# Kernel tuning notes

Measured on AMD Instinct MI355X. Metric: run time of the kernel, lower is better.

The kernel has to match this reference:

```python
import jax, jax.numpy as jnp
import numpy as np

B, T, D, H, E, L = 128, 200, 256, 4, 4, 2
HD = D // H
ITEM = 50000


def _ln(x, s, b):
    m = x.mean(-1, keepdims=True)
    v = ((x - m) ** 2).mean(-1, keepdims=True)
    return (x - m) / jnp.sqrt(v + 1e-8) * s + b


def setup_inputs() -> dict:
    key = jax.random.key(0)
    ks = jax.random.split(key, 20)
    n = lambda k, sh: jax.random.normal(k, sh, jnp.float32) * 0.02
    inp = {}
    inp['log_seqs'] = jax.random.randint(ks[0], (B, T), 0, ITEM + 1)
    inp['pos_seqs'] = jax.random.randint(ks[1], (B, T), 0, ITEM + 1)
    inp['neg_seqs'] = jax.random.randint(ks[2], (B, T), 0, ITEM + 1)
    inp['expert_ids'] = jax.random.randint(ks[3], (B,), 0, E)
    inp['item_emb'] = n(ks[4], (ITEM + 1, D)).at[0].set(0.0)  # padding_idx=0
    inp['pos_emb'] = n(ks[5], (T + 1, D)).at[0].set(0.0)
    inp['attn_ln_s'] = jnp.ones((L, D), jnp.float32)
    inp['attn_ln_b'] = jnp.zeros((L, D), jnp.float32)
    inp['in_w'] = n(ks[6], (L, E, 3 * D, D))
    inp['in_b'] = jnp.zeros((L, E, 3 * D), jnp.float32)
    inp['out_w'] = n(ks[7], (L, E, D, D))
    inp['out_b'] = jnp.zeros((L, E, D), jnp.float32)
    inp['fwd_ln_s'] = jnp.ones((L, D), jnp.float32)
    inp['fwd_ln_b'] = jnp.zeros((L, D), jnp.float32)
    inp['ffn_w1'] = n(ks[8], (L, D, D))
    inp['ffn_b1'] = jnp.zeros((L, D), jnp.float32)
    inp['ffn_w2'] = n(ks[9], (L, D, D))
    inp['ffn_b2'] = jnp.zeros((L, D), jnp.float32)
    inp['last_ln_s'] = jnp.ones((D,), jnp.float32)
    inp['last_ln_b'] = jnp.zeros((D,), jnp.float32)
    return inp


def reference(log_seqs, pos_seqs, neg_seqs, expert_ids, item_emb, pos_emb,
              attn_ln_s, attn_ln_b, in_w, in_b, out_w, out_b,
              fwd_ln_s, fwd_ln_b, ffn_w1, ffn_b1, ffn_w2, ffn_b2,
              last_ln_s, last_ln_b):
    seqs = item_emb[log_seqs] * jnp.float32(np.sqrt(D))          # [B,T,D]
    poss = jnp.arange(1, T + 1)[None, :] * (log_seqs != 0)       # pos ids, 0 where pad
    seqs = seqs + pos_emb[poss]
    causal = jnp.tril(jnp.ones((T, T), bool))
    scale = jnp.float32(1.0 / np.sqrt(HD))

    for l in range(L):
        qn = _ln(seqs, attn_ln_s[l], attn_ln_b[l])               # query is LN'd; K,V are not
        wq, wk, wv = in_w[l, :, :D], in_w[l, :, D:2 * D], in_w[l, :, 2 * D:]
        bq, bk, bv = in_b[l, :, :D], in_b[l, :, D:2 * D], in_b[l, :, 2 * D:]
        q = jnp.einsum('btd,efd->ebtf', qn, wq) + bq[:, None, None, :]
        k = jnp.einsum('btd,efd->ebtf', seqs, wk) + bk[:, None, None, :]
        v = jnp.einsum('btd,efd->ebtf', seqs, wv) + bv[:, None, None, :]
        q = q.reshape(E, B, T, H, HD)
        k = k.reshape(E, B, T, H, HD)
        v = v.reshape(E, B, T, H, HD)
        scores = jnp.einsum('ebqhd,ebkhd->ebhqk', q, k) * scale  # [E,B,H,T,T]
        scores = jnp.where(causal, scores, jnp.float32(-1e9))
        attn = jax.nn.softmax(scores, axis=-1)
        o = jnp.einsum('ebhqk,ebkhd->ebqhd', attn, v).reshape(E, B, T, D)
        o = jnp.einsum('ebtd,efd->ebtf', o, out_w[l]) + out_b[l][:, None, None, :]
        gated = o[expert_ids, jnp.arange(B)]                     # hard one-hot gate -> [B,T,D]
        seqs = qn + gated
        seqs = _ln(seqs, fwd_ln_s[l], fwd_ln_b[l])
        h = jax.nn.relu(seqs @ ffn_w1[l].T + ffn_b1[l])
        seqs = seqs + (h @ ffn_w2[l].T + ffn_b2[l])

    feats = _ln(seqs, last_ln_s, last_ln_b)                      # [B,T,D]
    pos_logits = (feats * item_emb[pos_seqs]).sum(-1)            # [B,T]
    neg_logits = (feats * item_emb[neg_seqs]).sum(-1)
    return (pos_logits, neg_logits)
```

## Files before the change

### kernel.cpp

```cpp
#include <hip/hip_runtime.h>
#include <hip/hip_bf16.h>

namespace {

typedef unsigned short ushort;
constexpr int B  = 128;
constexpr int T  = 200;
constexpr int D  = 256;
constexpr int H  = 4;
constexpr int NE = 4;
constexpr int NL = 2;
constexpr int HD = 64;
constexpr int BT = B * T;

constexpr int BM = 64;
constexpr int BK = 64;
constexpr int MT = (T + BM - 1) / BM;
constexpr int HS = 264;

typedef __bf16 bf16x8 __attribute__((ext_vector_type(8)));
typedef float f32x4 __attribute__((ext_vector_type(4)));
typedef unsigned short ushort8v __attribute__((ext_vector_type(8)));

__device__ inline float wave_sum(float x) {
#pragma unroll
  for (int off = 32; off > 0; off >>= 1) x += __shfl_xor(x, off);
  return x;
}
__device__ inline unsigned int f2bf(float x) {
  unsigned int u = __float_as_uint(x);
  return (u + 0x7fffu + ((u >> 16) & 1u)) >> 16;
}
__device__ inline ushort f2bfs(float x) { return (ushort)f2bf(x); }
__device__ inline float bf2f(ushort u) {
  return __uint_as_float((unsigned int)u << 16);
}
__device__ inline bf16x8 ldb8(const ushort* p) {
  return __builtin_bit_cast(bf16x8, *(const ushort8v*)p);
}

__global__ void k_cvt(const float* __restrict__ src, ushort* __restrict__ dst,
                      int n4) {
  int i = blockIdx.x * 256 + threadIdx.x;
  if (i < n4) {
    float4 v = ((const float4*)src)[i];
    ushort4 u;
    u.x = f2bfs(v.x); u.y = f2bfs(v.y); u.z = f2bfs(v.z); u.w = f2bfs(v.w);
    ((ushort4*)dst)[i] = u;
  }
}

__global__ __launch_bounds__(256) void k_embed_ln(
    const int* __restrict__ log_seqs, const float* __restrict__ item_emb,
    const float* __restrict__ pos_emb, const float* __restrict__ lns,
    const float* __restrict__ lnb, ushort* __restrict__ seqs,
    ushort* __restrict__ qn) {
  int tok = blockIdx.x * 4 + (threadIdx.x >> 6);
  int lane = threadIdx.x & 63;
  int t = tok % T;
  int idx = log_seqs[tok];
  int pos = (idx != 0) ? (t + 1) : 0;
  float4 iv = ((const float4*)(item_emb + (size_t)idx * D))[lane];
  float4 pv = ((const float4*)(pos_emb + (size_t)pos * D))[lane];
  float v0 = iv.x * 16.0f + pv.x;
  float v1 = iv.y * 16.0f + pv.y;
  float v2 = iv.z * 16.0f + pv.z;
  float v3 = iv.w * 16.0f + pv.w;
  ushort4 r;
  r.x = f2bfs(v0); r.y = f2bfs(v1); r.z = f2bfs(v2); r.w = f2bfs(v3);
  ((ushort4*)(seqs + (size_t)tok * D))[lane] = r;
  float mean = wave_sum(v0 + v1 + v2 + v3) * (1.0f / D);
  float c0 = v0 - mean, c1 = v1 - mean, c2 = v2 - mean, c3 = v3 - mean;
  float var = wave_sum(c0 * c0 + c1 * c1 + c2 * c2 + c3 * c3) * (1.0f / D);
  float inv = rsqrtf(var + 1e-8f);
  float4 sv = ((const float4*)lns)[lane];
  float4 bv = ((const float4*)lnb)[lane];
  ushort4 o;
  o.x = f2bfs(c0 * inv * sv.x + bv.x);
  o.y = f2bfs(c1 * inv * sv.y + bv.y);
  o.z = f2bfs(c2 * inv * sv.z + bv.z);
  o.w = f2bfs(c3 * inv * sv.w + bv.w);
  ((ushort4*)(qn + (size_t)tok * D))[lane] = o;
}

template <int ROWS>
__device__ inline void stage_bf16(const ushort* __restrict__ src, int ld,
                                  int valid, int k0, ushort* __restrict__ dst,
                                  int tid) {
#pragma unroll
  for (int p = 0; p < ROWS * 8 / 256; p++) {
    int slot = p * 256 + tid;
    int r = slot >> 3, s_st = slot & 7;
    int s_src = s_st ^ (r & 7);
    int rs = (r < valid) ? r : (valid - 1);
    uint4 w = *(const uint4*)(src + (size_t)rs * ld + k0 + s_src * 8);
    *(uint4*)(dst + r * BK + s_st * 8) = w;
  }
}
__device__ inline bf16x8 frag(const ushort* tile, int row, int slot_log) {
  int s = slot_log ^ (row & 7);
  return ldb8(tile + row * BK + s * 8);
}

__global__ __launch_bounds__(256) void k_gemm_qkv(
    const ushort* __restrict__ qn, const ushort* __restrict__ seqs,
    const ushort* __restrict__ w, const float* __restrict__ bias,
    const int* __restrict__ expert_ids,
    ushort* __restrict__ q, ushort* __restrict__ k, ushort* __restrict__ v) {
  constexpr int NWG = B * MT * 6;
  int phys = blockIdx.x;
  int bid = (phys & 7) * (NWG >> 3) + (phys >> 3);
  int nt = bid % 6;
  int mt = (bid / 6) % MT;
  int b  = bid / (6 * MT);
  int e = expert_ids[b];
  int m0 = mt * BM;
  int valid = min(BM, T - m0);
  const ushort* X = (nt < 2) ? qn : seqs;
  const ushort* Xb = X + (size_t)(b * T + m0) * D;
  const ushort* Wb = w + (size_t)e * 3 * D * D + (size_t)nt * 128 * D;

  __shared__ __align__(16) ushort Xl[BM * BK];
  __shared__ __align__(16) ushort Wl[128 * BK];
  int tid = threadIdx.x, wv = tid >> 6, lane = tid & 63;
  int g = lane >> 4, lm = lane & 15;

  f32x4 acc[4][2];
#pragma unroll
  for (int mi = 0; mi < 4; mi++)
#pragma unroll
    for (int ni = 0; ni < 2; ni++) acc[mi][ni] = (f32x4){0.f, 0.f, 0.f, 0.f};

  for (int kt = 0; kt < D / BK; kt++) {
    stage_bf16<BM>(Xb, D, valid, kt * BK, Xl, tid);
    stage_bf16<128>(Wb, D, 128, kt * BK, Wl, tid);
    __syncthreads();
    bf16x8 a[4][2], bb[2][2];
#pragma unroll
    for (int mi = 0; mi < 4; mi++)
#pragma unroll
      for (int hh = 0; hh < 2; hh++)
        a[mi][hh] = frag(Xl, mi * 16 + lm, hh * 4 + g);
#pragma unroll
    for (int ni = 0; ni < 2; ni++)
#pragma unroll
      for (int hh = 0; hh < 2; hh++)
        bb[ni][hh] = frag(Wl, wv * 32 + ni * 16 + lm, hh * 4 + g);
#pragma unroll
    for (int mi = 0; mi < 4; mi++)
#pragma unroll
      for (int ni = 0; ni < 2; ni++) {
        acc[mi][ni] = __builtin_amdgcn_mfma_f32_16x16x32_bf16(a[mi][0], bb[ni][0],
                                                              acc[mi][ni], 0, 0, 0);
        acc[mi][ni] = __builtin_amdgcn_mfma_f32_16x16x32_bf16(a[mi][1], bb[ni][1],
                                                              acc[mi][ni], 0, 0, 0);
      }
    __syncthreads();
  }

  ushort* outb = (nt < 2) ? q : (nt < 4 ? k : v);
  size_t rowbase = (size_t)(b * T + m0);
#pragma unroll
  for (int mi = 0; mi < 4; mi++) {
#pragma unroll
    for (int ni = 0; ni < 2; ni++) {
      int col = (nt & 1) * 128 + wv * 32 + ni * 16 + lm;
      float bbv = bias[e * 3 * D + nt * 128 + wv * 32 + ni * 16 + lm];
#pragma unroll
      for (int r = 0; r < 4; r++) {
        int lr = mi * 16 + 4 * g + r;
        if (lr < valid)
          outb[(rowbase + lr) * D + col] = f2bfs(acc[mi][ni][r] + bbv);
      }
    }
  }
}

__global__ __launch_bounds__(256) void k_oproj(
    const ushort* __restrict__ o, const ushort* __restrict__ qn,
    const ushort* __restrict__ w, const float* __restrict__ bo,
    const float* __restrict__ lns, const float* __restrict__ lnb,
    const int* __restrict__ expert_ids, ushort* __restrict__ seqs) {
  int bid = blockIdx.x;
  int mt = bid % MT;
  int b  = bid / MT;
  int e = expert_ids[b];
  int m0 = mt * BM;
  int valid = min(BM, T - m0);
  const ushort* Xb = o + (size_t)(b * T + m0) * D;
  const ushort* Wb = w + (size_t)e * D * D;

  __shared__ __align__(16) ushort Xl[BM * BK];
  __shared__ __align__(16) ushort Wl[D * BK];
  __shared__ float rs_sum[BM][4];
  __shared__ float rs_sq[BM][4];
  int tid = threadIdx.x, wv = tid >> 6, lane = tid & 63;
  int g = lane >> 4, lm = lane & 15;

  f32x4 acc[4][4];
#pragma unroll
  for (int mi = 0; mi < 4; mi++)
#pragma unroll
    for (int ni = 0; ni < 4; ni++) acc[mi][ni] = (f32x4){0.f, 0.f, 0.f, 0.f};

  for (int kt = 0; kt < D / BK; kt++) {
    stage_bf16<BM>(Xb, D, valid, kt * BK, Xl, tid);
    stage_bf16<D>(Wb, D, D, kt * BK, Wl, tid);
    __syncthreads();
    bf16x8 a[4][2], bb[4][2];
#pragma unroll
    for (int mi = 0; mi < 4; mi++)
#pragma unroll
      for (int hh = 0; hh < 2; hh++)
        a[mi][hh] = frag(Xl, mi * 16 + lm, hh * 4 + g);
#pragma unroll
    for (int ni = 0; ni < 4; ni++)
#pragma unroll
      for (int hh = 0; hh < 2; hh++)
        bb[ni][hh] = frag(Wl, wv * 64 + ni * 16 + lm, hh * 4 + g);
#pragma unroll
    for (int mi = 0; mi < 4; mi++)
#pragma unroll
      for (int ni = 0; ni < 4; ni++) {
        acc[mi][ni] = __builtin_amdgcn_mfma_f32_16x16x32_bf16(a[mi][0], bb[ni][0],
                                                              acc[mi][ni], 0, 0, 0);
        acc[mi][ni] = __builtin_amdgcn_mfma_f32_16x16x32_bf16(a[mi][1], bb[ni][1],
                                                              acc[mi][ni], 0, 0, 0);
      }
    __syncthreads();
  }

  size_t rowbase = (size_t)(b * T + m0);
#pragma unroll
  for (int ni = 0; ni < 4; ni++) {
    int col = wv * 64 + ni * 16 + lm;
    float bbv = bo[e * D + col];
#pragma unroll
    for (int mi = 0; mi < 4; mi++)
#pragma unroll
      for (int r = 0; r < 4; r++) {
        int lr = mi * 16 + 4 * g + r;
        int lrc = (lr < valid) ? lr : (valid - 1);
        acc[mi][ni][r] += bbv + bf2f(qn[(rowbase + lrc) * D + col]);
      }
  }
#pragma unroll
  for (int mi = 0; mi < 4; mi++)
#pragma unroll
    for (int r = 0; r < 4; r++) {
      float s = 0.f, q2 = 0.f;
#pragma unroll
      for (int ni = 0; ni < 4; ni++) {
        float x = acc[mi][ni][r];
        s += x; q2 += x * x;
      }
#pragma unroll
      for (int off = 1; off < 16; off <<= 1) {
        s += __shfl_xor(s, off);
        q2 += __shfl_xor(q2, off);
      }
      if (lm == 0) {
        int row = mi * 16 + 4 * g + r;
        rs_sum[row][wv] = s;
        rs_sq[row][wv] = q2;
      }
    }
  __syncthreads();
  float scv[4], bcv[4];
#pragma unroll
  for (int ni = 0; ni < 4; ni++) {
    int col = wv * 64 + ni * 16 + lm;
    scv[ni] = lns[col];
    bcv[ni] = lnb[col];
  }
#pragma unroll
  for (int mi = 0; mi < 4; mi++)
#pragma unroll
    for (int r = 0; r < 4; r++) {
      int lr = mi * 16 + 4 * g + r;
      float4 s4 = *(const float4*)rs_sum[lr];
      float4 q4 = *(const float4*)rs_sq[lr];
      float mean = (s4.x + s4.y + s4.z + s4.w) * (1.0f / D);
      float var = (q4.x + q4.y + q4.z + q4.w) * (1.0f / D) - mean * mean;
      float rstd = rsqrtf(fmaxf(var, 0.f) + 1e-8f);
      if (lr < valid) {
#pragma unroll
        for (int ni = 0; ni < 4; ni++) {
          int col = wv * 64 + ni * 16 + lm;
          float lnv = (acc[mi][ni][r] - mean) * rstd * scv[ni] + bcv[ni];
          seqs[(rowbase + lr) * D + col] = f2bfs(lnv);
        }
      }
    }
}

__global__ __launch_bounds__(256) void k_ffn(
    const ushort* __restrict__ xin, const ushort* __restrict__ w1,
    const float* __restrict__ b1, const ushort* __restrict__ w2,
    const float* __restrict__ b2, const float* __restrict__ lns,
    const float* __restrict__ lnb, ushort* __restrict__ seqs,
    ushort* __restrict__ qn) {
  int bid = blockIdx.x;
  int mt = bid % MT;
  int b  = bid / MT;
  int m0 = mt * BM;
  int valid = min(BM, T - m0);
  const ushort* Xb = xin + (size_t)(b * T + m0) * D;

  __shared__ __align__(16) ushort Xl[BM * BK];
  __shared__ __align__(16) ushort Wl[D * BK];
  __shared__ __align__(16) ushort hl[BM * HS];
  __shared__ float rs_sum[BM][4];
  __shared__ float rs_sq[BM][4];
  int tid = threadIdx.x, wv = tid >> 6, lane = tid & 63;
  int g = lane >> 4, lm = lane & 15;
  size_t rowbase = (size_t)(b * T + m0);

  f32x4 acc[4][4];
#pragma unroll
  for (int mi = 0; mi < 4; mi++)
#pragma unroll
    for (int ni = 0; ni < 4; ni++) acc[mi][ni] = (f32x4){0.f, 0.f, 0.f, 0.f};

  for (int kt = 0; kt < D / BK; kt++) {
    stage_bf16<BM>(Xb, D, valid, kt * BK, Xl, tid);
    stage_bf16<D>(w1, D, D, kt * BK, Wl, tid);
    __syncthreads();
    bf16x8 a[4][2], bb[4][2];
#pragma unroll
    for (int mi = 0; mi < 4; mi++)
#pragma unroll
      for (int hh = 0; hh < 2; hh++)
        a[mi][hh] = frag(Xl, mi * 16 + lm, hh * 4 + g);
#pragma unroll
    for (int ni = 0; ni < 4; ni++)
#pragma unroll
      for (int hh = 0; hh < 2; hh++)
        bb[ni][hh] = frag(Wl, wv * 64 + ni * 16 + lm, hh * 4 + g);
#pragma unroll
    for (int mi = 0; mi < 4; mi++)
#pragma unroll
      for (int ni = 0; ni < 4; ni++) {
        acc[mi][ni] = __builtin_amdgcn_mfma_f32_16x16x32_bf16(a[mi][0], bb[ni][0],
                                                              acc[mi][ni], 0, 0, 0);
        acc[mi][ni] = __builtin_amdgcn_mfma_f32_16x16x32_bf16(a[mi][1], bb[ni][1],
                                                              acc[mi][ni], 0, 0, 0);
      }
    __syncthreads();
  }
#pragma unroll
  for (int ni = 0; ni < 4; ni++) {
    int col = wv * 64 + ni * 16 + lm;
    float bbv = b1[col];
#pragma unroll
    for (int mi = 0; mi < 4; mi++)
#pragma unroll
      for (int r = 0; r < 4; r++) {
        int row = mi * 16 + 4 * g + r;
        hl[row * HS + col] = f2bfs(fmaxf(acc[mi][ni][r] + bbv, 0.f));
      }
  }
#pragma unroll
  for (int mi = 0; mi < 4; mi++)
#pragma unroll
    for (int ni = 0; ni < 4; ni++) acc[mi][ni] = (f32x4){0.f, 0.f, 0.f, 0.f};
  for (int kt = 0; kt < D / BK; kt++) {
    stage_bf16<D>(w2, D, D, kt * BK, Wl, tid);
    __syncthreads();
    bf16x8 a[4][2], bb[4][2];
#pragma unroll
    for (int mi = 0; mi < 4; mi++)
#pragma unroll
      for (int hh = 0; hh < 2; hh++)
        a[mi][hh] = ldb8(&hl[(mi * 16 + lm) * HS + kt * BK + hh * 32 + 8 * g]);
#pragma unroll
    for (int ni = 0; ni < 4; ni++)
#pragma unroll
      for (int hh = 0; hh < 2; hh++)
        bb[ni][hh] = frag(Wl, wv * 64 + ni * 16 + lm, hh * 4 + g);
#pragma unroll
    for (int mi = 0; mi < 4; mi++)
#pragma unroll
      for (int ni = 0; ni < 4; ni++) {
        acc[mi][ni] = __builtin_amdgcn_mfma_f32_16x16x32_bf16(a[mi][0], bb[ni][0],
                                                              acc[mi][ni], 0, 0, 0);
        acc[mi][ni] = __builtin_amdgcn_mfma_f32_16x16x32_bf16(a[mi][1], bb[ni][1],
                                                              acc[mi][ni], 0, 0, 0);
      }
    __syncthreads();
  }
#pragma unroll
  for (int ni = 0; ni < 4; ni++) {
    int col = wv * 64 + ni * 16 + lm;
    float bbv = b2[col];
#pragma unroll
    for (int mi = 0; mi < 4; mi++)
#pragma unroll
      for (int r = 0; r < 4; r++) {
        int lr = mi * 16 + 4 * g + r;
        int lrc = (lr < valid) ? lr : (valid - 1);
        acc[mi][ni][r] += bbv + bf2f(xin[(rowbase + lrc) * D + col]);
      }
  }
#pragma unroll
  for (int mi = 0; mi < 4; mi++)
#pragma unroll
    for (int r = 0; r < 4; r++) {
      float s = 0.f, q2 = 0.f;
#pragma unroll
      for (int ni = 0; ni < 4; ni++) {
        float x = acc[mi][ni][r];
        s += x; q2 += x * x;
      }
#pragma unroll
      for (int off = 1; off < 16; off <<= 1) {
        s += __shfl_xor(s, off);
        q2 += __shfl_xor(q2, off);
      }
      if (lm == 0) {
        int row = mi * 16 + 4 * g + r;
        rs_sum[row][wv] = s;
        rs_sq[row][wv] = q2;
      }
    }
  __syncthreads();
  float scv[4], bcv[4];
#pragma unroll
  for (int ni = 0; ni < 4; ni++) {
    int col = wv * 64 + ni * 16 + lm;
    scv[ni] = lns[col];
    bcv[ni] = lnb[col];
  }
#pragma unroll
  for (int mi = 0; mi < 4; mi++)
#pragma unroll
    for (int r = 0; r < 4; r++) {
      int lr = mi * 16 + 4 * g + r;
      float4 s4 = *(const float4*)rs_sum[lr];
      float4 q4 = *(const float4*)rs_sq[lr];
      float mean = (s4.x + s4.y + s4.z + s4.w) * (1.0f / D);
      float var = (q4.x + q4.y + q4.z + q4.w) * (1.0f / D) - mean * mean;
      float rstd = rsqrtf(fmaxf(var, 0.f) + 1e-8f);
      if (lr < valid) {
#pragma unroll
        for (int ni = 0; ni < 4; ni++) {
          int col = wv * 64 + ni * 16 + lm;
          float val = acc[mi][ni][r];
          size_t idx = (rowbase + lr) * D + col;
          seqs[idx] = f2bfs(val);
          qn[idx] = f2bfs((val - mean) * rstd * scv[ni] + bcv[ni]);
        }
      }
    }
}

constexpr int KROWS = 224;
constexpr int KSS = 72;
constexpr int VSS = 232;
constexpr int PSS = 40;
__global__ __launch_bounds__(256) void k_attn(const ushort* __restrict__ q,
                                              const ushort* __restrict__ k,
                                              const ushort* __restrict__ v,
                                              ushort* __restrict__ o) {
  int bh = blockIdx.x;
  int b = bh >> 2, h = bh & 3;
  __shared__ __align__(16) ushort Kl[KROWS][KSS];
  __shared__ __align__(16) ushort Vt[HD][VSS];
  __shared__ __align__(16) ushort Pl[4][16][PSS];
  const size_t base = (size_t)b * T * D + h * HD;
  int tid = threadIdx.x, wave = tid >> 6, lane = tid & 63;
  int g = lane >> 4, lm = lane & 15;

#pragma unroll
  for (int p = 0; p < 7; p++) {
    int slot = p * 256 + tid;
    int key = slot >> 3, s8 = (slot & 7) << 3;
    uint4 w = make_uint4(0, 0, 0, 0);
    if (key < T) w = *(const uint4*)(k + base + (size_t)key * D + s8);
    *(uint4*)&Kl[key][s8] = w;
  }
#pragma unroll
  for (int p = 0; p < 28; p++) {
    int slot = p * 256 + tid;
    int key = slot >> 5, dp = (slot & 31) << 1;
    unsigned int w = 0;
    if (key < T) w = *(const unsigned int*)(v + base + (size_t)key * D + dp);
    Vt[dp][key] = (ushort)(w & 0xffffu);
    Vt[dp + 1][key] = (ushort)(w >> 16);
  }
  __syncthreads();

  const unsigned long long SCHED = 0x0189D27AD36BD45CULL;
  unsigned sch = (unsigned)(SCHED >> (wave * 16)) & 0xFFFFu;
  const float sc = 0.125f * 1.44269504f;

  for (int si = 0; si < 4; si++) {
    int qt = (sch >> (si * 4)) & 15;
    if (qt > 12) break;
    int row = qt * 16 + lm;
    int qrow = min(row, T - 1);
    const ushort* qr = q + base + (size_t)qrow * D;
    bf16x8 qf0 = ldb8(qr + 8 * g);
    bf16x8 qf1 = ldb8(qr + 32 + 8 * g);

    f32x4 oacc[4];
#pragma unroll
    for (int dt = 0; dt < 4; dt++) oacc[dt] = (f32x4){0.f, 0.f, 0.f, 0.f};
    float mrun = -3e38f, lsum = 0.f;

    int nch = qt / 2 + 1;
    for (int c = 0; c < nch; c++) {
      int kb = c * 32;
      f32x4 s01[2];
#pragma unroll
      for (int t = 0; t < 2; t++) {
        int krow = kb + t * 16 + lm;
        bf16x8 a0 = ldb8(&Kl[krow][8 * g]);
        bf16x8 a1 = ldb8(&Kl[krow][32 + 8 * g]);
        f32x4 z = (f32x4){0.f, 0.f, 0.f, 0.f};
        z = __builtin_amdgcn_mfma_f32_16x16x32_bf16(a0, qf0, z, 0, 0, 0);
        z = __builtin_amdgcn_mfma_f32_16x16x32_bf16(a1, qf1, z, 0, 0, 0);
        s01[t] = z;
      }
      float sv[8];
      float mx = -3e38f;
#pragma unroll
      for (int t = 0; t < 2; t++)
#pragma unroll
        for (int r = 0; r < 4; r++) {
          int key = kb + t * 16 + 4 * g + r;
          float x = (key <= row) ? s01[t][r] * sc : -3e38f;
          sv[t * 4 + r] = x;
          mx = fmaxf(mx, x);
        }
      mx = fmaxf(mx, __shfl_xor(mx, 16));
      mx = fmaxf(mx, __shfl_xor(mx, 32));
      float mnew = fmaxf(mrun, mx);
      float corr = __builtin_amdgcn_exp2f(mrun - mnew);
      float ps = 0.f;
      ushort8v pu;
#pragma unroll
      for (int i = 0; i < 8; i++) {
        float p = __builtin_amdgcn_exp2f(sv[i] - mnew);
        ps += p;
        pu[i] = f2bfs(p);
      }
      ps += __shfl_xor(ps, 16);
      ps += __shfl_xor(ps, 32);
      lsum = lsum * corr + ps;
      mrun = mnew;
      *(ushort4*)&Pl[wave][lm][4 * g]      = ((ushort4*)&pu)[0];
      *(ushort4*)&Pl[wave][lm][16 + 4 * g] = ((ushort4*)&pu)[1];
#pragma unroll
      for (int dt = 0; dt < 4; dt++)
#pragma unroll
        for (int r = 0; r < 4; r++) oacc[dt][r] *= corr;
      bf16x8 pf = ldb8(&Pl[wave][lm][8 * g]);
#pragma unroll
      for (int dt = 0; dt < 4; dt++) {
        bf16x8 av = ldb8(&Vt[dt * 16 + lm][kb + 8 * g]);
        oacc[dt] = __builtin_amdgcn_mfma_f32_16x16x32_bf16(av, pf, oacc[dt], 0, 0, 0);
      }
    }

    if (row < T) {
      float rinv = 1.0f / lsum;
      ushort* orow = o + base + (size_t)row * D;
#pragma unroll
      for (int dt = 0; dt < 4; dt++) {
        ushort4 uo;
        uo.x = f2bfs(oacc[dt][0] * rinv);
        uo.y = f2bfs(oacc[dt][1] * rinv);
        uo.z = f2bfs(oacc[dt][2] * rinv);
        uo.w = f2bfs(oacc[dt][3] * rinv);
        *(ushort4*)(orow + dt * 16 + 4 * g) = uo;
      }
    }
  }
}

__global__ __launch_bounds__(256) void k_final(const ushort* __restrict__ seqs,
                                               const float* __restrict__ sc,
                                               const float* __restrict__ bi,
                                               const int* __restrict__ pos_seqs,
                                               const int* __restrict__ neg_seqs,
                                               const float* __restrict__ item_emb,
                                               float* __restrict__ out) {
  int tok = blockIdx.x * 4 + (threadIdx.x >> 6);
  int lane = threadIdx.x & 63;
  ushort4 xu = ((const ushort4*)(seqs + (size_t)tok * D))[lane];
  float x0 = bf2f(xu.x), x1 = bf2f(xu.y), x2 = bf2f(xu.z), x3 = bf2f(xu.w);
  float mean = wave_sum(x0 + x1 + x2 + x3) * (1.0f / D);
  float c0 = x0 - mean, c1 = x1 - mean, c2 = x2 - mean, c3 = x3 - mean;
  float var = wave_sum(c0 * c0 + c1 * c1 + c2 * c2 + c3 * c3) * (1.0f / D);
  float inv = rsqrtf(var + 1e-8f);
  float4 sv = ((const float4*)sc)[lane];
  float4 bv = ((const float4*)bi)[lane];
  float f0 = c0 * inv * sv.x + bv.x;
  float f1 = c1 * inv * sv.y + bv.y;
  float f2 = c2 * inv * sv.z + bv.z;
  float f3 = c3 * inv * sv.w + bv.w;
  int ip = pos_seqs[tok];
  int in_ = neg_seqs[tok];
  float4 pe = ((const float4*)(item_emb + (size_t)ip * D))[lane];
  float4 ne = ((const float4*)(item_emb + (size_t)in_ * D))[lane];
  float dp = wave_sum(f0 * pe.x + f1 * pe.y + f2 * pe.z + f3 * pe.w);
  float dn = wave_sum(f0 * ne.x + f1 * ne.y + f2 * ne.z + f3 * ne.w);
  if (lane == 0) {
    out[tok] = dp;
    out[BT + tok] = dn;
  }
}

}

extern "C" void kernel_launch(void* const* d_in, const int* in_sizes, int n_in,
                              void* d_out, int out_size, void* d_ws, size_t ws_size,
                              hipStream_t stream) {
  const int*   log_seqs   = (const int*)d_in[0];
  const int*   pos_seqs   = (const int*)d_in[1];
  const int*   neg_seqs   = (const int*)d_in[2];
  const int*   expert_ids = (const int*)d_in[3];
  const float* item_emb   = (const float*)d_in[4];
  const float* pos_emb    = (const float*)d_in[5];
  const float* attn_ln_s  = (const float*)d_in[6];
  const float* attn_ln_b  = (const float*)d_in[7];
  const float* in_w       = (const float*)d_in[8];
  const float* in_b       = (const float*)d_in[9];
  const float* out_w      = (const float*)d_in[10];
  const float* out_b      = (const float*)d_in[11];
  const float* fwd_ln_s   = (const float*)d_in[12];
  const float* fwd_ln_b   = (const float*)d_in[13];
  const float* ffn_w1     = (const float*)d_in[14];
  const float* ffn_b1     = (const float*)d_in[15];
  const float* ffn_w2     = (const float*)d_in[16];
  const float* ffn_b2     = (const float*)d_in[17];
  const float* last_ln_s  = (const float*)d_in[18];
  const float* last_ln_b  = (const float*)d_in[19];
  float* out = (float*)d_out;

  const size_t N = (size_t)BT * D;
  ushort* seqs = (ushort*)d_ws;
  ushort* qn   = seqs + N;
  ushort* q    = qn + N;
  ushort* kbuf = q + N;
  ushort* vbuf = kbuf + N;
  ushort* obuf = kbuf;
  ushort* wqkv = vbuf + N;
  ushort* wout = wqkv + (size_t)NL * NE * 3 * D * D;
  ushort* wf1  = wout + (size_t)NL * NE * D * D;
  ushort* wf2  = wf1 + (size_t)NL * D * D;

  {
    int n4a = NL * NE * 3 * D * D / 4;
    int n4b = NL * NE * D * D / 4;
    int n4c = NL * D * D / 4;
    k_cvt<<<(n4a + 255) / 256, 256, 0, stream>>>(in_w, wqkv, n4a);
    k_cvt<<<(n4b + 255) / 256, 256, 0, stream>>>(out_w, wout, n4b);
    k_cvt<<<(n4c + 255) / 256, 256, 0, stream>>>(ffn_w1, wf1, n4c);
    k_cvt<<<(n4c + 255) / 256, 256, 0, stream>>>(ffn_w2, wf2, n4c);
  }

  k_embed_ln<<<BT / 4, 256, 0, stream>>>(log_seqs, item_emb, pos_emb,
                                         attn_ln_s, attn_ln_b, seqs, qn);

  for (int l = 0; l < NL; l++) {
    int ln_next = (l + 1 < NL) ? (l + 1) : l;
    k_gemm_qkv<<<B * MT * 6, 256, 0, stream>>>(
        qn, seqs, wqkv + (size_t)l * NE * 3 * D * D,
        in_b + (size_t)l * NE * 3 * D, expert_ids, q, kbuf, vbuf);
    k_attn<<<B * H, 256, 0, stream>>>(q, kbuf, vbuf, obuf);
    k_oproj<<<B * MT, 256, 0, stream>>>(
        obuf, qn, wout + (size_t)l * NE * D * D, out_b + (size_t)l * NE * D,
        fwd_ln_s + (size_t)l * D, fwd_ln_b + (size_t)l * D, expert_ids, seqs);
    k_ffn<<<B * MT, 256, 0, stream>>>(
        seqs, wf1 + (size_t)l * D * D, ffn_b1 + (size_t)l * D,
        wf2 + (size_t)l * D * D, ffn_b2 + (size_t)l * D,
        attn_ln_s + (size_t)ln_next * D, attn_ln_b + (size_t)ln_next * D,
        seqs, qn);
  }

  k_final<<<BT / 4, 256, 0, stream>>>(seqs, last_ln_s, last_ln_b, pos_seqs,
                                      neg_seqs, item_emb, out);
}
```

Before: 261.7 us.

## Use 8-wave blocks with register-prefetched K tiles in GEMM and attention kernels

After: 313.1 us. 1.2x slower.

```diff
diff --git a/kernel.cpp b/kernel.cpp
--- a/kernel.cpp
+++ b/kernel.cpp
@@ -84,17 +84,25 @@
 }
 
 template <int ROWS>
-__device__ inline void stage_bf16(const ushort* __restrict__ src, int ld,
-                                  int valid, int k0, ushort* __restrict__ dst,
-                                  int tid) {
-#pragma unroll
-  for (int p = 0; p < ROWS * 8 / 256; p++) {
-    int slot = p * 256 + tid;
+__device__ inline void stage_ld(const ushort* __restrict__ src, int ld,
+                                int valid, int k0, uint4* regs, int tid) {
+#pragma unroll
+  for (int p = 0; p < ROWS * 8 / 512; p++) {
+    int slot = p * 512 + tid;
     int r = slot >> 3, s_st = slot & 7;
     int s_src = s_st ^ (r & 7);
     int rs = (r < valid) ? r : (valid - 1);
-    uint4 w = *(const uint4*)(src + (size_t)rs * ld + k0 + s_src * 8);
-    *(uint4*)(dst + r * BK + s_st * 8) = w;
+    regs[p] = *(const uint4*)(src + (size_t)rs * ld + k0 + s_src * 8);
+  }
+}
+template <int ROWS>
+__device__ inline void stage_st(const uint4* regs, ushort* __restrict__ dst,
+                                int tid) {
+#pragma unroll
+  for (int p = 0; p < ROWS * 8 / 512; p++) {
+    int slot = p * 512 + tid;
+    int r = slot >> 3, s_st = slot & 7;
+    *(uint4*)(dst + r * BK + s_st * 8) = regs[p];
   }
 }
 __device__ inline bf16x8 frag(const ushort* tile, int row, int slot_log) {
@@ -102,7 +110,7 @@
   return ldb8(tile + row * BK + s * 8);
 }
 
-__global__ __launch_bounds__(256) void k_gemm_qkv(
+__global__ __launch_bounds__(512, 4) void k_gemm_qkv(
     const ushort* __restrict__ qn, const ushort* __restrict__ seqs,
     const ushort* __restrict__ w, const float* __restrict__ bias,
     const int* __restrict__ expert_ids,
@@ -123,31 +131,41 @@
   __shared__ __align__(16) ushort Xl[BM * BK];
   __shared__ __align__(16) ushort Wl[128 * BK];
   int tid = threadIdx.x, wv = tid >> 6, lane = tid & 63;
+  int wr = wv >> 2, wc = wv & 3;
   int g = lane >> 4, lm = lane & 15;
 
-  f32x4 acc[4][2];
-#pragma unroll
-  for (int mi = 0; mi < 4; mi++)
+  f32x4 acc[2][2];
+#pragma unroll
+  for (int mi = 0; mi < 2; mi++)
 #pragma unroll
     for (int ni = 0; ni < 2; ni++) acc[mi][ni] = (f32x4){0.f, 0.f, 0.f, 0.f};
 
+  uint4 xr[1], wrg[2];
+  stage_ld<BM>(Xb, D, valid, 0, xr, tid);
+  stage_ld<128>(Wb, D, 128, 0, wrg, tid);
+  stage_st<BM>(xr, Xl, tid);
+  stage_st<128>(wrg, Wl, tid);
+  __syncthreads();
+
+#pragma unroll
   for (int kt = 0; kt < D / BK; kt++) {
-    stage_bf16<BM>(Xb, D, valid, kt * BK, Xl, tid);
-    stage_bf16<128>(Wb, D, 128, kt * BK, Wl, tid);
-    __syncthreads();
-    bf16x8 a[4][2], bb[2][2];
-#pragma unroll
-    for (int mi = 0; mi < 4; mi++)
+    if (kt < D / BK - 1) {
+      stage_ld<BM>(Xb, D, valid, (kt + 1) * BK, xr, tid);
+      stage_ld<128>(Wb, D, 128, (kt + 1) * BK, wrg, tid);
+    }
+    bf16x8 a[2][2], bb[2][2];
+#pragma unroll
+    for (int mi = 0; mi < 2; mi++)
 #pragma unroll
       for (int hh = 0; hh < 2; hh++)
-        a[mi][hh] = frag(Xl, mi * 16 + lm, hh * 4 + g);
+        a[mi][hh] = frag(Xl, wr * 32 + mi * 16 + lm, hh * 4 + g);
 #pragma unroll
     for (int ni = 0; ni < 2; ni++)
 #pragma unroll
       for (int hh = 0; hh < 2; hh++)
-        bb[ni][hh] = frag(Wl, wv * 32 + ni * 16 + lm, hh * 4 + g);
-#pragma unroll
-    for (int mi = 0; mi < 4; mi++)
+        bb[ni][hh] = frag(Wl, wc * 32 + ni * 16 + lm, hh * 4 + g);
+#pragma unroll
+    for (int mi = 0; mi < 2; mi++)
 #pragma unroll
       for (int ni = 0; ni < 2; ni++) {
         acc[mi][ni] = __builtin_amdgcn_mfma_f32_16x16x32_bf16(a[mi][0], bb[ni][0],
@@ -156,19 +174,24 @@
                                                               acc[mi][ni], 0, 0, 0);
       }
     __syncthreads();
+    if (kt < D / BK - 1) {
+      stage_st<BM>(xr, Xl, tid);
+      stage_st<128>(wrg, Wl, tid);
+      __syncthreads();
+    }
   }
 
   ushort* outb = (nt < 2) ? q : (nt < 4 ? k : v);
   size_t rowbase = (size_t)(b * T + m0);
 #pragma unroll
-  for (int mi = 0; mi < 4; mi++) {
+  for (int mi = 0; mi < 2; mi++) {
 #pragma unroll
     for (int ni = 0; ni < 2; ni++) {
-      int col = (nt & 1) * 128 + wv * 32 + ni * 16 + lm;
-      float bbv = bias[e * 3 * D + nt * 128 + wv * 32 + ni * 16 + lm];
+      int col = (nt & 1) * 128 + wc * 32 + ni * 16 + lm;
+      float bbv = bias[e * 3 * D + nt * 128 + wc * 32 + ni * 16 + lm];
 #pragma unroll
       for (int r = 0; r < 4; r++) {
-        int lr = mi * 16 + 4 * g + r;
+        int lr = wr * 32 + mi * 16 + 4 * g + r;
         if (lr < valid)
           outb[(rowbase + lr) * D + col] = f2bfs(acc[mi][ni][r] + bbv);
       }
@@ -176,7 +199,7 @@
   }
 }
 
-__global__ __launch_bounds__(256) void k_oproj(
+__global__ __launch_bounds__(512, 4) void k_oproj(
     const ushort* __restrict__ o, const ushort* __restrict__ qn,
     const ushort* __restrict__ w, const float* __restrict__ bo,
     const float* __restrict__ lns, const float* __restrict__ lnb,
@@ -195,31 +218,41 @@
   __shared__ float rs_sum[BM][4];
   __shared__ float rs_sq[BM][4];
   int tid = threadIdx.x, wv = tid >> 6, lane = tid & 63;
+  int wr = wv >> 2, wc = wv & 3;
   int g = lane >> 4, lm = lane & 15;
 
-  f32x4 acc[4][4];
-#pragma unroll
-  for (int mi = 0; mi < 4; mi++)
+  f32x4 acc[2][4];
+#pragma unroll
+  for (int mi = 0; mi < 2; mi++)
 #pragma unroll
     for (int ni = 0; ni < 4; ni++) acc[mi][ni] = (f32x4){0.f, 0.f, 0.f, 0.f};
 
+  uint4 xr[1], wrg[4];
+  stage_ld<BM>(Xb, D, valid, 0, xr, tid);
+  stage_ld<D>(Wb, D, D, 0, wrg, tid);
+  stage_st<BM>(xr, Xl, tid);
+  stage_st<D>(wrg, Wl, tid);
+  __syncthreads();
+
+#pragma unroll
   for (int kt = 0; kt < D / BK; kt++) {
-    stage_bf16<BM>(Xb, D, valid, kt * BK, Xl, tid);
-    stage_bf16<D>(Wb, D, D, kt * BK, Wl, tid);
-    __syncthreads();
-    bf16x8 a[4][2], bb[4][2];
-#pragma unroll
-    for (int mi = 0; mi < 4; mi++)
+    if (kt < D / BK - 1) {
+      stage_ld<BM>(Xb, D, valid, (kt + 1) * BK, xr, tid);
+      stage_ld<D>(Wb, D, D, (kt + 1) * BK, wrg, tid);
+    }
+    bf16x8 a[2][2], bb[4][2];
+#pragma unroll
+    for (int mi = 0; mi < 2; mi++)
 #pragma unroll
       for (int hh = 0; hh < 2; hh++)
-        a[mi][hh] = frag(Xl, mi * 16 + lm, hh * 4 + g);
+        a[mi][hh] = frag(Xl, wr * 32 + mi * 16 + lm, hh * 4 + g);
 #pragma unroll
     for (int ni = 0; ni < 4; ni++)
 #pragma unroll
       for (int hh = 0; hh < 2; hh++)
-        bb[ni][hh] = frag(Wl, wv * 64 + ni * 16 + lm, hh * 4 + g);
-#pragma unroll
-    for (int mi = 0; mi < 4; mi++)
+        bb[ni][hh] = frag(Wl, wc * 64 + ni * 16 + lm, hh * 4 + g);
+#pragma unroll
+    for (int mi = 0; mi < 2; mi++)
 #pragma unroll
       for (int ni = 0; ni < 4; ni++) {
         acc[mi][ni] = __builtin_amdgcn_mfma_f32_16x16x32_bf16(a[mi][0], bb[ni][0],
@@ -228,24 +261,29 @@
                                                               acc[mi][ni], 0, 0, 0);
       }
     __syncthreads();
+    if (kt < D / BK - 1) {
+      stage_st<BM>(xr, Xl, tid);
+      stage_st<D>(wrg, Wl, tid);
+      __syncthreads();
+    }
   }
 
   size_t rowbase = (size_t)(b * T + m0);
 #pragma unroll
   for (int ni = 0; ni < 4; ni++) {
-    int col = wv * 64 + ni * 16 + lm;
+    int col = wc * 64 + ni * 16 + lm;
     float bbv = bo[e * D + col];
 #pragma unroll
-    for (int mi = 0; mi < 4; mi++)
+    for (int mi = 0; mi < 2; mi++)
 #pragma unroll
       for (int r = 0; r < 4; r++) {
-        int lr = mi * 16 + 4 * g + r;
+        int lr = wr * 32 + mi * 16 + 4 * g + r;
         int lrc = (lr < valid) ? lr : (valid - 1);
         acc[mi][ni][r] += bbv + bf2f(qn[(rowbase + lrc) * D + col]);
       }
   }
 #pragma unroll
-  for (int mi = 0; mi < 4; mi++)
+  for (int mi = 0; mi < 2; mi++)
 #pragma unroll
     for (int r = 0; r < 4; r++) {
       float s = 0.f, q2 = 0.f;
@@ -260,24 +298,24 @@
         q2 += __shfl_xor(q2, off);
       }
       if (lm == 0) {
-        int row = mi * 16 + 4 * g + r;
-        rs_sum[row][wv] = s;
-        rs_sq[row][wv] = q2;
+        int row = wr * 32 + mi * 16 + 4 * g + r;
+        rs_sum[row][wc] = s;
+        rs_sq[row][wc] = q2;
       }
     }
   __syncthreads();
   float scv[4], bcv[4];
 #pragma unroll
   for (int ni = 0; ni < 4; ni++) {
-    int col = wv * 64 + ni * 16 + lm;
+    int col = wc * 64 + ni * 16 + lm;
     scv[ni] = lns[col];
     bcv[ni] = lnb[col];
   }
 #pragma unroll
-  for (int mi = 0; mi < 4; mi++)
+  for (int mi = 0; mi < 2; mi++)
 #pragma unroll
     for (int r = 0; r < 4; r++) {
-      int lr = mi * 16 + 4 * g + r;
+      int lr = wr * 32 + mi * 16 + 4 * g + r;
       float4 s4 = *(const float4*)rs_sum[lr];
       float4 q4 = *(const float4*)rs_sq[lr];
       float mean = (s4.x + s4.y + s4.z + s4.w) * (1.0f / D);
@@ -286,7 +324,7 @@
       if (lr < valid) {
 #pragma unroll
         for (int ni = 0; ni < 4; ni++) {
-          int col = wv * 64 + ni * 16 + lm;
+          int col = wc * 64 + ni * 16 + lm;
           float lnv = (acc[mi][ni][r] - mean) * rstd * scv[ni] + bcv[ni];
           seqs[(rowbase + lr) * D + col] = f2bfs(lnv);
         }
@@ -294,7 +332,7 @@
     }
 }
 
-__global__ __launch_bounds__(256) void k_ffn(
+__global__ __launch_bounds__(512, 4) void k_ffn(
     const ushort* __restrict__ xin, const ushort* __restrict__ w1,
     const float* __restrict__ b1, const ushort* __restrict__ w2,
     const float* __restrict__ b2, const float* __restrict__ lns,
@@ -313,32 +351,41 @@
   __shared__ float rs_sum[BM][4];
   __shared__ float rs_sq[BM][4];
   int tid = threadIdx.x, wv = tid >> 6, lane = tid & 63;
+  int wr = wv >> 2, wc = wv & 3;
   int g = lane >> 4, lm = lane & 15;
   size_t rowbase = (size_t)(b * T + m0);
 
-  f32x4 acc[4][4];
-#pragma unroll
-  for (int mi = 0; mi < 4; mi++)
+  f32x4 acc[2][4];
+#pragma unroll
+  for (int mi = 0; mi < 2; mi++)
 #pragma unroll
     for (int ni = 0; ni < 4; ni++) acc[mi][ni] = (f32x4){0.f, 0.f, 0.f, 0.f};
 
+  uint4 xr[1], wrg[4];
+  stage_ld<BM>(Xb, D, valid, 0, xr, tid);
+  stage_ld<D>(w1, D, D, 0, wrg, tid);
+  stage_st<BM>(xr, Xl, tid);
+  stage_st<D>(wrg, Wl, tid);
+  __syncthreads();
+#pragma unroll
   for (int kt = 0; kt < D / BK; kt++) {
-    stage_bf16<BM>(Xb, D, valid, kt * BK, Xl, tid);
-    stage_bf16<D>(w1, D, D, kt * BK, Wl, tid);
-    __syncthreads();
-    bf16x8 a[4][2], bb[4][2];
-#pragma unroll
-    for (int mi = 0; mi < 4; mi++)
+    if (kt < D / BK - 1) {
+      stage_ld<BM>(Xb, D, valid, (kt + 1) * BK, xr, tid);
+      stage_ld<D>(w1, D, D, (kt + 1) * BK, wrg, tid);
+    }
+    bf16x8 a[2][2], bb[4][2];
+#pragma unroll
+    for (int mi = 0; mi < 2; mi++)
 #pragma unroll
       for (int hh = 0; hh < 2; hh++)
-        a[mi][hh] = frag(Xl, mi * 16 + lm, hh * 4 + g);
+        a[mi][hh] = frag(Xl, wr * 32 + mi * 16 + lm, hh * 4 + g);
 #pragma unroll
     for (int ni = 0; ni < 4; ni++)
 #pragma unroll
       for (int hh = 0; hh < 2; hh++)
-        bb[ni][hh] = frag(Wl, wv * 64 + ni * 16 + lm, hh * 4 + g);
-#pragma unroll
-    for (int mi = 0; mi < 4; mi++)
+        bb[ni][hh] = frag(Wl, wc * 64 + ni * 16 + lm, hh * 4 + g);
+#pragma unroll
+    for (int mi = 0; mi < 2; mi++)
 #pragma unroll
       for (int ni = 0; ni < 4; ni++) {
         acc[mi][ni] = __builtin_amdgcn_mfma_f32_16x16x32_bf16(a[mi][0], bb[ni][0],
@@ -347,39 +394,48 @@
                                                               acc[mi][ni], 0, 0, 0);
       }
     __syncthreads();
-  }
+    if (kt < D / BK - 1) {
+      stage_st<BM>(xr, Xl, tid);
+      stage_st<D>(wrg, Wl, tid);
+      __syncthreads();
+    }
+  }
+  stage_ld<D>(w2, D, D, 0, wrg, tid);
 #pragma unroll
   for (int ni = 0; ni < 4; ni++) {
-    int col = wv * 64 + ni * 16 + lm;
+    int col = wc * 64 + ni * 16 + lm;
     float bbv = b1[col];
 #pragma unroll
-    for (int mi = 0; mi < 4; mi++)
+    for (int mi = 0; mi < 2; mi++)
 #pragma unroll
       for (int r = 0; r < 4; r++) {
-        int row = mi * 16 + 4 * g + r;
+        int row = wr * 32 + mi * 16 + 4 * g + r;
         hl[row * HS + col] = f2bfs(fmaxf(acc[mi][ni][r] + bbv, 0.f));
       }
   }
-#pragma unroll
-  for (int mi = 0; mi < 4; mi++)
+  stage_st<D>(wrg, Wl, tid);
+  __syncthreads();
+
+#pragma unroll
+  for (int mi = 0; mi < 2; mi++)
 #pragma unroll
     for (int ni = 0; ni < 4; ni++) acc[mi][ni] = (f32x4){0.f, 0.f, 0.f, 0.f};
+#pragma unroll
   for (int kt = 0; kt < D / BK; kt++) {
-    stage_bf16<D>(w2, D, D, kt * BK, Wl, tid);
-    __syncthreads();
-    bf16x8 a[4][2], bb[4][2];
-#pragma unroll
-    for (int mi = 0; mi < 4; mi++)
+    if (kt < D / BK - 1) stage_ld<D>(w2, D, D, (kt + 1) * BK, wrg, tid);
+    bf16x8 a[2][2], bb[4][2];
+#pragma unroll
+    for (int mi = 0; mi < 2; mi++)
 #pragma unroll
       for (int hh = 0; hh < 2; hh++)
-        a[mi][hh] = ldb8(&hl[(mi * 16 + lm) * HS + kt * BK + hh * 32 + 8 * g]);
+        a[mi][hh] = ldb8(&hl[(wr * 32 + mi * 16 + lm) * HS + kt * BK + hh * 32 + 8 * g]);
 #pragma unroll
     for (int ni = 0; ni < 4; ni++)
 #pragma unroll
       for (int hh = 0; hh < 2; hh++)
-        bb[ni][hh] = frag(Wl, wv * 64 + ni * 16 + lm, hh * 4 + g);
-#pragma unroll
-    for (int mi = 0; mi < 4; mi++)
+        bb[ni][hh] = frag(Wl, wc * 64 + ni * 16 + lm, hh * 4 + g);
+#pragma unroll
+    for (int mi = 0; mi < 2; mi++)
 #pragma unroll
       for (int ni = 0; ni < 4; ni++) {
         acc[mi][ni] = __builtin_amdgcn_mfma_f32_16x16x32_bf16(a[mi][0], bb[ni][0],
@@ -388,22 +444,26 @@
                                                               acc[mi][ni], 0, 0, 0);
       }
     __syncthreads();
+    if (kt < D / BK - 1) {
+      stage_st<D>(wrg, Wl, tid);
+      __syncthreads();
+    }
   }
 #pragma unroll
   for (int ni = 0; ni < 4; ni++) {
-    int col = wv * 64 + ni * 16 + lm;
+    int col = wc * 64 + ni * 16 + lm;
     float bbv = b2[col];
 #pragma unroll
-    for (int mi = 0; mi < 4; mi++)
+    for (int mi = 0; mi < 2; mi++)
 #pragma unroll
       for (int r = 0; r < 4; r++) {
-        int lr = mi * 16 + 4 * g + r;
+        int lr = wr * 32 + mi * 16 + 4 * g + r;
         int lrc = (lr < valid) ? lr : (valid - 1);
         acc[mi][ni][r] += bbv + bf2f(xin[(rowbase + lrc) * D + col]);
       }
   }
 #pragma unroll
-  for (int mi = 0; mi < 4; mi++)
+  for (int mi = 0; mi < 2; mi++)
 #pragma unroll
     for (int r = 0; r < 4; r++) {
       float s = 0.f, q2 = 0.f;
@@ -418,24 +478,24 @@
         q2 += __shfl_xor(q2, off);
       }
       if (lm == 0) {
-        int row = mi * 16 + 4 * g + r;
-        rs_sum[row][wv] = s;
-        rs_sq[row][wv] = q2;
+        int row = wr * 32 + mi * 16 + 4 * g + r;
+        rs_sum[row][wc] = s;
+        rs_sq[row][wc] = q2;
       }
     }
   __syncthreads();
   float scv[4], bcv[4];
 #pragma unroll
   for (int ni = 0; ni < 4; ni++) {
-    int col = wv * 64 + ni * 16 + lm;
+    int col = wc * 64 + ni * 16 + lm;
     scv[ni] = lns[col];
     bcv[ni] = lnb[col];
   }
 #pragma unroll
-  for (int mi = 0; mi < 4; mi++)
+  for (int mi = 0; mi < 2; mi++)
 #pragma unroll
     for (int r = 0; r < 4; r++) {
-      int lr = mi * 16 + 4 * g + r;
+      int lr = wr * 32 + mi * 16 + 4 * g + r;
       float4 s4 = *(const float4*)rs_sum[lr];
       float4 q4 = *(const float4*)rs_sq[lr];
       float mean = (s4.x + s4.y + s4.z + s4.w) * (1.0f / D);
@@ -444,7 +504,7 @@
       if (lr < valid) {
 #pragma unroll
         for (int ni = 0; ni < 4; ni++) {
-          int col = wv * 64 + ni * 16 + lm;
+          int col = wc * 64 + ni * 16 + lm;
           float val = acc[mi][ni][r];
           size_t idx = (rowbase + lr) * D + col;
           seqs[idx] = f2bfs(val);
@@ -458,30 +518,32 @@
 constexpr int KSS = 72;
 constexpr int VSS = 232;
 constexpr int PSS = 40;
-__global__ __launch_bounds__(256) void k_attn(const ushort* __restrict__ q,
-                                              const ushort* __restrict__ k,
-                                              const ushort* __restrict__ v,
-                                              ushort* __restrict__ o) {
+__global__ __launch_bounds__(512, 4) void k_attn(const ushort* __restrict__ q,
+                                                 const ushort* __restrict__ k,
+                                                 const ushort* __restrict__ v,
+                                                 ushort* __restrict__ o) {
   int bh = blockIdx.x;
   int b = bh >> 2, h = bh & 3;
   __shared__ __align__(16) ushort Kl[KROWS][KSS];
   __shared__ __align__(16) ushort Vt[HD][VSS];
-  __shared__ __align__(16) ushort Pl[4][16][PSS];
+  __shared__ __align__(16) ushort Pl[8][16][PSS];
   const size_t base = (size_t)b * T * D + h * HD;
-  int tid = threadIdx.x, wave = tid >> 6, lane = tid & 63;
+  int tid = threadIdx.x, wv = tid >> 6, lane = tid & 63;
   int g = lane >> 4, lm = lane & 15;
 
 #pragma unroll
-  for (int p = 0; p < 7; p++) {
-    int slot = p * 256 + tid;
-    int key = slot >> 3, s8 = (slot & 7) << 3;
-    uint4 w = make_uint4(0, 0, 0, 0);
-    if (key < T) w = *(const uint4*)(k + base + (size_t)key * D + s8);
-    *(uint4*)&Kl[key][s8] = w;
-  }
-#pragma unroll
-  for (int p = 0; p < 28; p++) {
-    int slot = p * 256 + tid;
+  for (int p = 0; p < 4; p++) {
+    int slot = p * 512 + tid;
+    if (slot < KROWS * 8) {
+      int key = slot >> 3, s8 = (slot & 7) << 3;
+      uint4 w = make_uint4(0, 0, 0, 0);
+      if (key < T) w = *(const uint4*)(k + base + (size_t)key * D + s8);
+      *(uint4*)&Kl[key][s8] = w;
+    }
+  }
+#pragma unroll
+  for (int p = 0; p < 14; p++) {
+    int slot = p * 512 + tid;
     int key = slot >> 5, dp = (slot & 31) << 1;
     unsigned int w = 0;
     if (key < T) w = *(const unsigned int*)(v + base + (size_t)key * D + dp);
@@ -490,13 +552,13 @@
   }
   __syncthreads();
 
-  const unsigned long long SCHED = 0x0189D27AD36BD45CULL;
-  unsigned sch = (unsigned)(SCHED >> (wave * 16)) & 0xFFFFu;
+  unsigned sch = (((0xF543210Fu >> (wv * 4)) & 0xF) << 4) |
+                 ((0xF6789ABCu >> (wv * 4)) & 0xF);
   const float sc = 0.125f * 1.44269504f;
 
-  for (int si = 0; si < 4; si++) {
-    int qt = (sch >> (si * 4)) & 15;
-    if (qt > 12) break;
+  for (int si = 0; si < 2; si++) {
+    int qt = (sch >> (si * 4)) & 0xF;
+    if (qt == 0xF) continue;
     int row = qt * 16 + lm;
     int qrow = min(row, T - 1);
     const ushort* qr = q + base + (size_t)qrow * D;
@@ -549,13 +611,13 @@
       ps += __shfl_xor(ps, 32);
       lsum = lsum * corr + ps;
       mrun = mnew;
-      *(ushort4*)&Pl[wave][lm][4 * g]      = ((ushort4*)&pu)[0];
-      *(ushort4*)&Pl[wave][lm][16 + 4 * g] = ((ushort4*)&pu)[1];
+      *(ushort4*)&Pl[wv][lm][4 * g]      = ((ushort4*)&pu)[0];
+      *(ushort4*)&Pl[wv][lm][16 + 4 * g] = ((ushort4*)&pu)[1];
 #pragma unroll
       for (int dt = 0; dt < 4; dt++)
 #pragma unroll
         for (int r = 0; r < 4; r++) oacc[dt][r] *= corr;
-      bf16x8 pf = ldb8(&Pl[wave][lm][8 * g]);
+      bf16x8 pf = ldb8(&Pl[wv][lm][8 * g]);
 #pragma unroll
       for (int dt = 0; dt < 4; dt++) {
         bf16x8 av = ldb8(&Vt[dt * 16 + lm][kb + 8 * g]);
@@ -666,14 +728,14 @@
 
   for (int l = 0; l < NL; l++) {
     int ln_next = (l + 1 < NL) ? (l + 1) : l;
-    k_gemm_qkv<<<B * MT * 6, 256, 0, stream>>>(
+    k_gemm_qkv<<<B * MT * 6, 512, 0, stream>>>(
         qn, seqs, wqkv + (size_t)l * NE * 3 * D * D,
         in_b + (size_t)l * NE * 3 * D, expert_ids, q, kbuf, vbuf);
-    k_attn<<<B * H, 256, 0, stream>>>(q, kbuf, vbuf, obuf);
-    k_oproj<<<B * MT, 256, 0, stream>>>(
+    k_attn<<<B * H, 512, 0, stream>>>(q, kbuf, vbuf, obuf);
+    k_oproj<<<B * MT, 512, 0, stream>>>(
         obuf, qn, wout + (size_t)l * NE * D * D, out_b + (size_t)l * NE * D,
         fwd_ln_s + (size_t)l * D, fwd_ln_b + (size_t)l * D, expert_ids, seqs);
-    k_ffn<<<B * MT, 256, 0, stream>>>(
+    k_ffn<<<B * MT, 512, 0, stream>>>(
         seqs, wf1 + (size_t)l * D * D, ffn_b1 + (size_t)l * D,
         wf2 + (size_t)l * D * D, ffn_b2 + (size_t)l * D,
         attn_ln_s + (size_t)ln_next * D, attn_ln_b + (size_t)ln_next * D,
```
